# Kernel optimization log

Measured on AMD Instinct MI355X. Metric: run time of the kernel, lower is better.

The kernel has to match this reference:

```python
import jax, jax.numpy as jnp
import numpy as np

B, S, D = 128, 512, 512  # source requires S == hidden_dim for bmm(Q^T, K^T) to type-check


def setup_inputs() -> dict:
    key = jax.random.key(0)
    ks = jax.random.split(key, 7)
    scale = 1.0 / np.sqrt(D)
    return {
        "x": jax.random.normal(ks[0], (B, S, D), dtype=jnp.float32),
        "Wq": jax.random.uniform(ks[1], (D, D), jnp.float32, -scale, scale),
        "bq": jax.random.uniform(ks[2], (D,), jnp.float32, -scale, scale),
        "Wk": jax.random.uniform(ks[3], (D, D), jnp.float32, -scale, scale),
        "bk": jax.random.uniform(ks[4], (D,), jnp.float32, -scale, scale),
        "Wv": jax.random.uniform(ks[5], (D, D), jnp.float32, -scale, scale),
        "bv": jax.random.uniform(ks[6], (D,), jnp.float32, -scale, scale),
    }


def reference(x, Wq, bq, Wk, bk, Wv, bv):
    # nn.Linear: y = x @ W^T + b
    Q = jnp.einsum("bsd,ed->bse", x, Wq) + bq  # (B,S,D)
    K = jnp.einsum("bsd,ed->bse", x, Wk) + bk
    V = jnp.einsum("bsd,ed->bse", x, Wv) + bv
    Qp = jnp.transpose(Q, (0, 2, 1))  # (B,D,S)
    Kp = jnp.transpose(K, (0, 2, 1))  # (B,D,S); bmm needs S == D
    energy = jnp.matmul(Qp, Kp)       # (B,D,D) -- unscaled, as in source
    attention = jax.nn.softmax(energy, axis=2)
    Vp = jnp.transpose(V, (0, 2, 1))  # (B,D,S)
    context = jnp.matmul(attention, Vp)  # (B,D,S)
    return jnp.transpose(context, (0, 2, 1))  # (B,S,D)
```

## Files before the change

kernel.cpp:

```cpp
#include <hip/hip_runtime.h>
#include <hip/hip_bf16.h>


#define NDIM 512
#define NBATCH 128
constexpr size_t SD = (size_t)NDIM * NDIM;

typedef __attribute__((ext_vector_type(8))) short bf16x8;
typedef __attribute__((ext_vector_type(4))) float f32x4;

typedef const __attribute__((address_space(1))) unsigned int* gas_ptr;
typedef __attribute__((address_space(3))) unsigned int* las_ptr;

struct alignas(8) us4 { unsigned short x, y, z, w; };
struct alignas(4) us2 { unsigned short x, y; };

__device__ __forceinline__ void gl_lds16(const void* g, void* lds) {
    __builtin_amdgcn_global_load_lds((gas_ptr)g, (las_ptr)lds, 16, 0, 0);
}
__device__ __forceinline__ unsigned short f2bf(float x) {
    return __builtin_bit_cast(unsigned short, __float2bfloat16(x));
}
__device__ __forceinline__ float bf2f(unsigned short u) {
    return __bfloat162float(__builtin_bit_cast(__hip_bfloat16, u));
}

template<int NSEG, int EPI, int BIAS>
__global__ __launch_bounds__(512, 2) void gemm8_nt(
    const unsigned short* a0, const unsigned short* a1, const unsigned short* a2, long sA,
    const unsigned short* b0, const unsigned short* b1, const unsigned short* b2, long sB,
    void* c0v, void* c1v, long sC, const float* __restrict__ bias)
{
    constexpr int NTK = NSEG * 8;
    __shared__ unsigned short AS[2][256 * 64];
    __shared__ unsigned short BS[2][256 * 64];

    const int nwg = gridDim.x;
    int id = blockIdx.x;
    int wg = ((nwg & 7) == 0) ? ((id & 7) * (nwg >> 3) + (id >> 3)) : id;
    const int z  = wg >> 2;
    const int m0 = ((wg >> 1) & 1) * 256;
    const int n0 = (wg & 1) * 256;

    const int tid = threadIdx.x;
    const int l = tid & 63, w = tid >> 6;
    const int wr = w >> 2, wc = w & 3;

    const size_t zA = (size_t)z * sA + (size_t)m0 * NDIM;
    const size_t zB = (size_t)z * sB + (size_t)n0 * NDIM;

    const int srow = tid >> 3;
    const int scol = (((tid & 7) ^ ((tid >> 3) & 7)) << 3);
    const int ldst = tid * 8;

    auto segA = [&](int s) {
        const unsigned short* p = a0;
        if constexpr (NSEG > 1) { if (s == 1) p = a1; else if (s == 2) p = a2; }
        return p;
    };
    auto segB = [&](int s) {
        const unsigned short* p = b0;
        if constexpr (NSEG > 1) { if (s == 1) p = b1; else if (s == 2) p = b2; }
        return p;
    };
    auto stageA = [&](int kt, int H, int slot) {
        const int seg = kt >> 3, k0 = (kt & 7) << 6;
        const unsigned short* g = segA(seg) + zA;
        #pragma unroll
        for (int j = 0; j < 2; ++j)
            gl_lds16(g + (size_t)(H * 128 + j * 64 + srow) * NDIM + k0 + scol,
                     &AS[slot][H * 8192 + j * 4096 + ldst]);
    };
    auto stageB = [&](int kt, int H, int slot) {
        const int seg = kt >> 3, k0 = (kt & 7) << 6;
        const unsigned short* g = segB(seg) + zB;
        #pragma unroll
        for (int j = 0; j < 2; ++j)
            gl_lds16(g + (size_t)(H * 128 + j * 64 + srow) * NDIM + k0 + scol,
                     &BS[slot][H * 8192 + j * 4096 + ldst]);
    };

    auto readA = [&](int slot, int H, bf16x8 (&dst)[4][2]) {
        #pragma unroll
        for (int mi = 0; mi < 4; ++mi) {
            const int row = H * 128 + wr * 64 + mi * 16 + (l & 15);
            #pragma unroll
            for (int kk = 0; kk < 2; ++kk) {
                const int s16 = ((kk << 2) + (l >> 4)) ^ (l & 7);
                dst[mi][kk] = *(const bf16x8*)&AS[slot][row * 64 + s16 * 8];
            }
        }
    };
    auto readB = [&](int slot, int H, bf16x8 (&dst)[2][2]) {
        #pragma unroll
        for (int ni = 0; ni < 2; ++ni) {
            const int row = H * 128 + wc * 32 + ni * 16 + (l & 15);
            #pragma unroll
            for (int kk = 0; kk < 2; ++kk) {
                const int s16 = ((kk << 2) + (l >> 4)) ^ (l & 7);
                dst[ni][kk] = *(const bf16x8*)&BS[slot][row * 64 + s16 * 8];
            }
        }
    };
    auto mfma16 = [&](f32x4 (&ac)[4][2], const bf16x8 (&a)[4][2],
                      const bf16x8 (&b)[2][2]) {
        __builtin_amdgcn_s_setprio(1);
        #pragma unroll
        for (int mi = 0; mi < 4; ++mi)
            #pragma unroll
            for (int ni = 0; ni < 2; ++ni)
                #pragma unroll
                for (int kk = 0; kk < 2; ++kk)
                    ac[mi][ni] = __builtin_amdgcn_mfma_f32_16x16x32_bf16(
                        a[mi][kk], b[ni][kk], ac[mi][ni], 0, 0, 0);
        __builtin_amdgcn_s_setprio(0);
    };

    f32x4 acc[2][2][4][2] = {};

    stageA(0, 0, 0); stageB(0, 0, 0); stageB(0, 1, 0); stageA(0, 1, 0);

    for (int kt = 0; kt < NTK; ++kt) {
        const int cur = kt & 1, nxt = cur ^ 1;
        const int ktn = (kt + 1 < NTK) ? kt + 1 : kt;
        bf16x8 af[4][2], b0f[2][2], b1f[2][2];

        stageA(ktn, 0, nxt);
        asm volatile("s_waitcnt vmcnt(6)" ::: "memory");
        asm volatile("s_barrier" ::: "memory");
        readA(cur, 0, af); readB(cur, 0, b0f);
        asm volatile("s_waitcnt lgkmcnt(0)" ::: "memory");
        __builtin_amdgcn_sched_barrier(0);
        mfma16(acc[0][0], af, b0f);

        stageB(ktn, 0, nxt);
        asm volatile("s_waitcnt vmcnt(6)" ::: "memory");
        asm volatile("s_barrier" ::: "memory");
        readB(cur, 1, b1f);
        asm volatile("s_waitcnt lgkmcnt(0)" ::: "memory");
        __builtin_amdgcn_sched_barrier(0);
        mfma16(acc[0][1], af, b1f);

        stageB(ktn, 1, nxt);
        asm volatile("s_waitcnt vmcnt(6)" ::: "memory");
        asm volatile("s_barrier" ::: "memory");
        readA(cur, 1, af);
        asm volatile("s_waitcnt lgkmcnt(0)" ::: "memory");
        __builtin_amdgcn_sched_barrier(0);
        mfma16(acc[1][1], af, b1f);

        stageA(ktn, 1, nxt);
        asm volatile("s_waitcnt vmcnt(6)" ::: "memory");
        asm volatile("s_barrier" ::: "memory");
        __builtin_amdgcn_sched_barrier(0);
        mfma16(acc[1][0], af, b0f);
    }
    asm volatile("s_waitcnt vmcnt(0)" ::: "memory");

    const size_t zc = (size_t)z * sC;
    const int cr = (l >> 4) << 2;
    const int cc = l & 15;
    #pragma unroll
    for (int Qr = 0; Qr < 2; ++Qr) {
        #pragma unroll
        for (int Qc = 0; Qc < 2; ++Qc) {
            #pragma unroll
            for (int mi = 0; mi < 4; ++mi) {
                #pragma unroll
                for (int r = 0; r < 4; ++r) {
                    const int m = m0 + Qr * 128 + wr * 64 + mi * 16 + cr + r;
                    const float bm = (BIAS == 1) ? bias[m] : 0.0f;
                    #pragma unroll
                    for (int ni = 0; ni < 2; ++ni) {
                        const int n = n0 + Qc * 128 + wc * 32 + ni * 16 + cc;
                        float v = acc[Qr][Qc][mi][ni][r] + bm + ((BIAS == 2) ? bias[n] : 0.0f);
                        const size_t idx = zc + (size_t)m * NDIM + n;
                        if (EPI == 0) {
                            ((float*)c0v)[idx] = v;
                        } else if (EPI == 1) {
                            ((unsigned short*)c0v)[idx] = f2bf(v);
                        } else {
                            const unsigned short h = f2bf(v);
                            ((unsigned short*)c0v)[idx] = h;
                            ((unsigned short*)c1v)[idx] = f2bf(v - bf2f(h));
                        }
                    }
                }
            }
        }
    }
}

template<int NSEG, int EPI, int BIAS>
__global__ __launch_bounds__(256) void gemm_bf16_nt(
    const unsigned short* a0, const unsigned short* a1, const unsigned short* a2, long sA,
    const unsigned short* b0, const unsigned short* b1, const unsigned short* b2, long sB,
    void* c0v, void* c1v, long sC, const float* __restrict__ bias)
{
    __shared__ unsigned short As[128 * 64];
    __shared__ unsigned short Bs[128 * 64];

    const int z  = blockIdx.z;
    const int m0 = blockIdx.y * 128, n0 = blockIdx.x * 128;
    const int tid = threadIdx.x;
    const int l = tid & 63, w = tid >> 6;
    const int wr = w >> 1, wc = w & 1;

    const int srow = tid >> 3;
    const int scol = (tid & 7) << 3;
    unsigned short* ldsA = &As[tid * 8];
    unsigned short* ldsB = &Bs[tid * 8];

    f32x4 acc[4][4] = {};

    const unsigned short* Asegs[3] = {a0, a1, a2};
    const unsigned short* Bsegs[3] = {b0, b1, b2};

    #pragma unroll
    for (int s = 0; s < NSEG; ++s) {
        const unsigned short* Ab = Asegs[s] + (size_t)z * sA + (size_t)m0 * NDIM;
        const unsigned short* Bb = Bsegs[s] + (size_t)z * sB + (size_t)n0 * NDIM;
        for (int k0 = 0; k0 < NDIM; k0 += 64) {
            __syncthreads();
            #pragma unroll
            for (int i = 0; i < 4; ++i) {
                gl_lds16(Ab + (size_t)(srow + i * 32) * NDIM + k0 + scol, ldsA + i * 2048);
                gl_lds16(Bb + (size_t)(srow + i * 32) * NDIM + k0 + scol, ldsB + i * 2048);
            }
            __syncthreads();
            #pragma unroll
            for (int kk = 0; kk < 2; ++kk) {
                bf16x8 af[4], bfv[4];
                #pragma unroll
                for (int f = 0; f < 4; ++f) {
                    af[f]  = *(const bf16x8*)&As[(wr * 64 + f * 16 + (l & 15)) * 64 + kk * 32 + (l >> 4) * 8];
                    bfv[f] = *(const bf16x8*)&Bs[(wc * 64 + f * 16 + (l & 15)) * 64 + kk * 32 + (l >> 4) * 8];
                }
                #pragma unroll
                for (int mi = 0; mi < 4; ++mi)
                    #pragma unroll
                    for (int ni = 0; ni < 4; ++ni)
                        acc[mi][ni] = __builtin_amdgcn_mfma_f32_16x16x32_bf16(
                            af[mi], bfv[ni], acc[mi][ni], 0, 0, 0);
            }
        }
    }

    const size_t zc = (size_t)z * sC;
    const int cr = (l >> 4) << 2;
    const int cc = l & 15;
    #pragma unroll
    for (int mi = 0; mi < 4; ++mi) {
        #pragma unroll
        for (int r = 0; r < 4; ++r) {
            const int m = m0 + wr * 64 + mi * 16 + cr + r;
            const float bm = (BIAS == 1) ? bias[m] : 0.0f;
            #pragma unroll
            for (int ni = 0; ni < 4; ++ni) {
                const int n = n0 + wc * 64 + ni * 16 + cc;
                float v = acc[mi][ni][r] + bm + ((BIAS == 2) ? bias[n] : 0.0f);
                const size_t idx = zc + (size_t)m * NDIM + n;
                if (EPI == 0) {
                    ((float*)c0v)[idx] = v;
                } else if (EPI == 1) {
                    ((unsigned short*)c0v)[idx] = f2bf(v);
                } else {
                    const unsigned short h = f2bf(v);
                    ((unsigned short*)c0v)[idx] = h;
                    ((unsigned short*)c1v)[idx] = f2bf(v - bf2f(h));
                }
            }
        }
    }
}

__global__ __launch_bounds__(256) void softmax_bf16(
    const float* __restrict__ E, unsigned short* __restrict__ A)
{
    __shared__ float red[256];
    const float* p = E + (size_t)blockIdx.x * NDIM;
    unsigned short* q = A + (size_t)blockIdx.x * NDIM;
    const int t = threadIdx.x;

    const float2 v = *(const float2*)(p + 2 * t);
    red[t] = fmaxf(v.x, v.y);
    __syncthreads();
    for (int s = 128; s > 0; s >>= 1) {
        if (t < s) red[t] = fmaxf(red[t], red[t + s]);
        __syncthreads();
    }
    const float mx = red[0];
    __syncthreads();

    const float ex = __expf(v.x - mx), ey = __expf(v.y - mx);
    red[t] = ex + ey;
    __syncthreads();
    for (int s = 128; s > 0; s >>= 1) {
        if (t < s) red[t] += red[t + s];
        __syncthreads();
    }
    const float inv = 1.0f / red[0];
    us2 o; o.x = f2bf(ex * inv); o.y = f2bf(ey * inv);
    *(us2*)(q + 2 * t) = o;
}

template<bool LO>
__global__ __launch_bounds__(256) void split_to_bf16(
    const float* __restrict__ src,
    unsigned short* __restrict__ hi, unsigned short* __restrict__ lo, int n4)
{
    const int i = blockIdx.x * 256 + threadIdx.x;
    if (i >= n4) return;
    const float4 v = ((const float4*)src)[i];
    us4 h;
    h.x = f2bf(v.x); h.y = f2bf(v.y); h.z = f2bf(v.z); h.w = f2bf(v.w);
    ((us4*)hi)[i] = h;
    if (LO) {
        us4 g;
        g.x = f2bf(v.x - bf2f(h.x)); g.y = f2bf(v.y - bf2f(h.y));
        g.z = f2bf(v.z - bf2f(h.z)); g.w = f2bf(v.w - bf2f(h.w));
        ((us4*)lo)[i] = g;
    }
}

extern "C" void kernel_launch(void* const* d_in, const int* in_sizes, int n_in,
                              void* d_out, int out_size, void* d_ws, size_t ws_size,
                              hipStream_t stream)
{
    const float* x  = (const float*)d_in[0];
    const float* Wq = (const float*)d_in[1];
    const float* bq = (const float*)d_in[2];
    const float* Wk = (const float*)d_in[3];
    const float* bk = (const float*)d_in[4];
    const float* Wv = (const float*)d_in[5];
    const float* bv = (const float*)d_in[6];
    float* out = (float*)d_out;

    long units = (long)(ws_size / (2 * SD));
    long cl = (units - 6) / 10;
    if (cl < 1) cl = 1;
    int c = 1;
    while (c * 2 <= cl && c < 128) c *= 2;
    const bool use8 = (c >= 64);
    if (!use8 && c > 32) c = 32;

    unsigned short* p = (unsigned short*)d_ws;
    auto take = [&](size_t elems) { unsigned short* r = p; p += elems; return r; };
    unsigned short* WqH = take(SD);
    unsigned short* WqL = take(SD);
    unsigned short* WkH = take(SD);
    unsigned short* WkL = take(SD);
    unsigned short* WvH = take(SD);
    unsigned short* xH  = take((size_t)c * SD);
    unsigned short* xL  = take((size_t)c * SD);
    unsigned short* QH  = take((size_t)c * SD);
    unsigned short* QL  = take((size_t)c * SD);
    unsigned short* KH  = take((size_t)c * SD);
    unsigned short* KL  = take((size_t)c * SD);
    unsigned short* Vb  = take((size_t)c * SD);
    unsigned short* Ab  = take((size_t)c * SD);
    float* Ew = (float*)p;

    const int n4w = (int)(SD / 4);
    split_to_bf16<true ><<<dim3((n4w + 255) / 256), dim3(256), 0, stream>>>(Wq, WqH, WqL, n4w);
    split_to_bf16<true ><<<dim3((n4w + 255) / 256), dim3(256), 0, stream>>>(Wk, WkH, WkL, n4w);
    split_to_bf16<false><<<dim3((n4w + 255) / 256), dim3(256), 0, stream>>>(Wv, WvH, nullptr, n4w);

    for (int b0 = 0; b0 < NBATCH; b0 += c) {
        const int cb = (NBATCH - b0 < c) ? (NBATCH - b0) : c;
        const int n4 = (int)((size_t)cb * SD / 4);
        split_to_bf16<true><<<dim3((n4 + 255) / 256), dim3(256), 0, stream>>>(
            x + (size_t)b0 * SD, xH, xL, n4);

        if (use8) {
            const dim3 g(4 * cb), blk(512);
            gemm8_nt<3, 2, 1><<<g, blk, 0, stream>>>(
                WqH, WqL, WqH, 0,  xH, xH, xL, (long)SD,  QH, QL, (long)SD, bq);
            gemm8_nt<3, 2, 2><<<g, blk, 0, stream>>>(
                xH, xL, xH, (long)SD,  WkH, WkH, WkL, 0,  KH, KL, (long)SD, bk);
            gemm8_nt<1, 1, 2><<<g, blk, 0, stream>>>(
                xH, nullptr, nullptr, (long)SD,  WvH, nullptr, nullptr, 0,  Vb, nullptr, (long)SD, bv);
            gemm8_nt<3, 0, 0><<<g, blk, 0, stream>>>(
                QH, QL, QH, (long)SD,  KH, KH, KL, (long)SD,  Ew, nullptr, (long)SD, nullptr);
            softmax_bf16<<<dim3(cb * NDIM), dim3(256), 0, stream>>>(Ew, Ab);
            gemm8_nt<1, 0, 0><<<g, blk, 0, stream>>>(
                Vb, nullptr, nullptr, (long)SD,  Ab, nullptr, nullptr, (long)SD,
                out + (size_t)b0 * SD, nullptr, (long)SD, nullptr);
        } else {
            const dim3 g(4, 4, cb), blk(256);
            gemm_bf16_nt<3, 2, 1><<<g, blk, 0, stream>>>(
                WqH, WqL, WqH, 0,  xH, xH, xL, (long)SD,  QH, QL, (long)SD, bq);
            gemm_bf16_nt<3, 2, 2><<<g, blk, 0, stream>>>(
                xH, xL, xH, (long)SD,  WkH, WkH, WkL, 0,  KH, KL, (long)SD, bk);
            gemm_bf16_nt<1, 1, 2><<<g, blk, 0, stream>>>(
                xH, nullptr, nullptr, (long)SD,  WvH, nullptr, nullptr, 0,  Vb, nullptr, (long)SD, bv);
            gemm_bf16_nt<3, 0, 0><<<g, blk, 0, stream>>>(
                QH, QL, QH, (long)SD,  KH, KH, KL, (long)SD,  Ew, nullptr, (long)SD, nullptr);
            softmax_bf16<<<dim3(cb * NDIM), dim3(256), 0, stream>>>(Ew, Ab);
            gemm_bf16_nt<1, 0, 0><<<g, blk, 0, stream>>>(
                Vb, nullptr, nullptr, (long)SD,  Ab, nullptr, nullptr, (long)SD,
                out + (size_t)b0 * SD, nullptr, (long)SD, nullptr);
        }
    }
}
```

Before: 607.7 us.

## Prefetch LDS fragments across k-steps in gemm8 and use wave-per-row softmax

The 8-wave GEMM main loop is reordered so the A0/B0 LDS fragment reads for the next k-tile are issued at the end of the current iteration. Partial lgkmcnt waits replace the full waits, so LDS reads can overlap MFMA work. The softmax kernel now gives each row to one wavefront, using float4 loads and shuffle reductions in place of shared-memory tree reductions with many __syncthreads, and launches a quarter as many blocks. The hand-tuned waitcnt counts add a risk of subtle correctness or hazard issues in the pipelined GEMM.

```diff
diff --git a/kernel.cpp b/kernel.cpp
--- a/kernel.cpp
+++ b/kernel.cpp
@@ -117,45 +117,48 @@
     };
 
     f32x4 acc[2][2][4][2] = {};
+    bf16x8 a0f[4][2], a1f[4][2], b0f[2][2], b1f[2][2];
 
     stageA(0, 0, 0); stageB(0, 0, 0); stageB(0, 1, 0); stageA(0, 1, 0);
+    asm volatile("s_waitcnt vmcnt(4)" ::: "memory");
+    asm volatile("s_barrier" ::: "memory");
+    readA(0, 0, a0f); readB(0, 0, b0f);
 
     for (int kt = 0; kt < NTK; ++kt) {
         const int cur = kt & 1, nxt = cur ^ 1;
         const int ktn = (kt + 1 < NTK) ? kt + 1 : kt;
-        bf16x8 af[4][2], b0f[2][2], b1f[2][2];
-
-        stageA(ktn, 0, nxt);
-        asm volatile("s_waitcnt vmcnt(6)" ::: "memory");
-        asm volatile("s_barrier" ::: "memory");
-        readA(cur, 0, af); readB(cur, 0, b0f);
-        asm volatile("s_waitcnt lgkmcnt(0)" ::: "memory");
-        __builtin_amdgcn_sched_barrier(0);
-        mfma16(acc[0][0], af, b0f);
-
-        stageB(ktn, 0, nxt);
+
+        stageA(ktn, 0, nxt); stageB(ktn, 0, nxt);
         asm volatile("s_waitcnt vmcnt(6)" ::: "memory");
         asm volatile("s_barrier" ::: "memory");
         readB(cur, 1, b1f);
-        asm volatile("s_waitcnt lgkmcnt(0)" ::: "memory");
+        asm volatile("s_waitcnt lgkmcnt(4)" ::: "memory");
         __builtin_amdgcn_sched_barrier(0);
-        mfma16(acc[0][1], af, b1f);
+        mfma16(acc[0][0], a0f, b0f);
 
         stageB(ktn, 1, nxt);
         asm volatile("s_waitcnt vmcnt(6)" ::: "memory");
         asm volatile("s_barrier" ::: "memory");
-        readA(cur, 1, af);
-        asm volatile("s_waitcnt lgkmcnt(0)" ::: "memory");
+        readA(cur, 1, a1f);
+        asm volatile("s_waitcnt lgkmcnt(8)" ::: "memory");
         __builtin_amdgcn_sched_barrier(0);
-        mfma16(acc[1][1], af, b1f);
+        mfma16(acc[0][1], a0f, b1f);
 
         stageA(ktn, 1, nxt);
         asm volatile("s_waitcnt vmcnt(6)" ::: "memory");
         asm volatile("s_barrier" ::: "memory");
+        asm volatile("s_waitcnt lgkmcnt(0)" ::: "memory");
         __builtin_amdgcn_sched_barrier(0);
-        mfma16(acc[1][0], af, b0f);
-    }
-    asm volatile("s_waitcnt vmcnt(0)" ::: "memory");
+        mfma16(acc[1][1], a1f, b1f);
+
+        asm volatile("s_waitcnt vmcnt(4)" ::: "memory");
+        asm volatile("s_barrier" ::: "memory");
+        __builtin_amdgcn_sched_barrier(0);
+        mfma16(acc[1][0], a1f, b0f);
+        __builtin_amdgcn_sched_barrier(0);
+        readA(nxt, 0, a0f); readB(nxt, 0, b0f);
+    }
+    asm volatile("s_waitcnt vmcnt(0) lgkmcnt(0)" ::: "memory");
 
     const size_t zc = (size_t)z * sC;
     const int cr = (l >> 4) << 2;
@@ -277,31 +280,36 @@
 __global__ __launch_bounds__(256) void softmax_bf16(
     const float* __restrict__ E, unsigned short* __restrict__ A)
 {
-    __shared__ float red[256];
-    const float* p = E + (size_t)blockIdx.x * NDIM;
-    unsigned short* q = A + (size_t)blockIdx.x * NDIM;
-    const int t = threadIdx.x;
-
-    const float2 v = *(const float2*)(p + 2 * t);
-    red[t] = fmaxf(v.x, v.y);
-    __syncthreads();
-    for (int s = 128; s > 0; s >>= 1) {
-        if (t < s) red[t] = fmaxf(red[t], red[t + s]);
-        __syncthreads();
-    }
-    const float mx = red[0];
-    __syncthreads();
-
-    const float ex = __expf(v.x - mx), ey = __expf(v.y - mx);
-    red[t] = ex + ey;
-    __syncthreads();
-    for (int s = 128; s > 0; s >>= 1) {
-        if (t < s) red[t] += red[t + s];
-        __syncthreads();
-    }
-    const float inv = 1.0f / red[0];
-    us2 o; o.x = f2bf(ex * inv); o.y = f2bf(ey * inv);
-    *(us2*)(q + 2 * t) = o;
+    const int l  = threadIdx.x & 63;
+    const int wv = threadIdx.x >> 6;
+    const size_t row = (size_t)blockIdx.x * 4 + wv;
+    const float* p = E + row * NDIM;
+    unsigned short* q = A + row * NDIM;
+
+    const float4 v0 = ((const float4*)p)[l * 2];
+    const float4 v1 = ((const float4*)p)[l * 2 + 1];
+
+    float mx = fmaxf(fmaxf(fmaxf(v0.x, v0.y), fmaxf(v0.z, v0.w)),
+                     fmaxf(fmaxf(v1.x, v1.y), fmaxf(v1.z, v1.w)));
+    #pragma unroll
+    for (int s = 32; s > 0; s >>= 1) mx = fmaxf(mx, __shfl_xor(mx, s, 64));
+
+    float e0 = __expf(v0.x - mx), e1 = __expf(v0.y - mx);
+    float e2 = __expf(v0.z - mx), e3 = __expf(v0.w - mx);
+    float e4 = __expf(v1.x - mx), e5 = __expf(v1.y - mx);
+    float e6 = __expf(v1.z - mx), e7 = __expf(v1.w - mx);
+    float sm = ((e0 + e1) + (e2 + e3)) + ((e4 + e5) + (e6 + e7));
+    #pragma unroll
+    for (int s = 32; s > 0; s >>= 1) sm += __shfl_xor(sm, s, 64);
+
+    const float inv = 1.0f / sm;
+    us4 o0, o1;
+    o0.x = f2bf(e0 * inv); o0.y = f2bf(e1 * inv);
+    o0.z = f2bf(e2 * inv); o0.w = f2bf(e3 * inv);
+    o1.x = f2bf(e4 * inv); o1.y = f2bf(e5 * inv);
+    o1.z = f2bf(e6 * inv); o1.w = f2bf(e7 * inv);
+    ((us4*)q)[l * 2]     = o0;
+    ((us4*)q)[l * 2 + 1] = o1;
 }
 
 template<bool LO>
@@ -382,7 +390,7 @@
                 xH, nullptr, nullptr, (long)SD,  WvH, nullptr, nullptr, 0,  Vb, nullptr, (long)SD, bv);
             gemm8_nt<3, 0, 0><<<g, blk, 0, stream>>>(
                 QH, QL, QH, (long)SD,  KH, KH, KL, (long)SD,  Ew, nullptr, (long)SD, nullptr);
-            softmax_bf16<<<dim3(cb * NDIM), dim3(256), 0, stream>>>(Ew, Ab);
+            softmax_bf16<<<dim3(cb * NDIM / 4), dim3(256), 0, stream>>>(Ew, Ab);
             gemm8_nt<1, 0, 0><<<g, blk, 0, stream>>>(
                 Vb, nullptr, nullptr, (long)SD,  Ab, nullptr, nullptr, (long)SD,
                 out + (size_t)b0 * SD, nullptr, (long)SD, nullptr);
@@ -396,7 +404,7 @@
                 xH, nullptr, nullptr, (long)SD,  WvH, nullptr, nullptr, 0,  Vb, nullptr, (long)SD, bv);
             gemm_bf16_nt<3, 0, 0><<<g, blk, 0, stream>>>(
                 QH, QL, QH, (long)SD,  KH, KH, KL, (long)SD,  Ew, nullptr, (long)SD, nullptr);
-            softmax_bf16<<<dim3(cb * NDIM), dim3(256), 0, stream>>>(Ew, Ab);
+            softmax_bf16<<<dim3(cb * NDIM / 4), dim3(256), 0, stream>>>(Ew, Ab);
             gemm_bf16_nt<1, 0, 0><<<g, blk, 0, stream>>>(
                 Vb, nullptr, nullptr, (long)SD,  Ab, nullptr, nullptr, (long)SD,
                 out + (size_t)b0 * SD, nullptr, (long)SD, nullptr);
```

Result: slower. 1.496 ms (+146.1%).
